# Kernel tuning notes

Measured on AMD Instinct MI355X. Metric: run time of the kernel, lower is better.

## Reference

```python
import jax, jax.numpy as jnp
import numpy as np

B, S, D, H, KS, VS, O = 4, 2048, 1024, 16, 64, 64, 1024


def setup_inputs() -> dict:
    key = jax.random.key(0)
    ks = jax.random.split(key, 11)
    def w(k, shp):
        return jax.random.normal(k, shp, dtype=jnp.float32) * 0.02
    return {
        "Q": jax.random.normal(ks[0], (B, S, D), dtype=jnp.float32),
        "K": jax.random.normal(ks[1], (B, S, D), dtype=jnp.float32),
        "V": jax.random.normal(ks[2], (B, S, D), dtype=jnp.float32),
        # per-head projection weights stacked over heads (equivalent to 3*H separate nn.Linear)
        "Wq": w(ks[3], (H, D, KS)), "bq": w(ks[4], (H, KS)),
        "Wk": w(ks[5], (H, D, KS)), "bk": w(ks[6], (H, KS)),
        "Wv": w(ks[7], (H, D, VS)), "bv": w(ks[8], (H, VS)),
        "Wo": w(ks[9], (H * VS, O)), "bo": w(ks[10], (O,)),
    }


def reference(Q, K, V, Wq, bq, Wk, bk, Wv, bv, Wo, bo):
    scale = jnp.sqrt(jnp.asarray(KS, dtype=Q.dtype))
    # per-head linear projections (vectorized over heads)
    q = jnp.einsum('bsd,hdk->bhsk', Q, Wq) + bq[:, None, :]   # [B,H,S,KS]
    k = jnp.einsum('bsd,hdk->bhsk', K, Wk) + bk[:, None, :]   # [B,H,S,KS]
    v = jnp.einsum('bsd,hdv->bhsv', V, Wv) + bv[:, None, :]   # [B,H,S,VS]
    # scaled dot-product attention, full S x S scores per head
    scores = jnp.einsum('bhsk,bhtk->bhst', q, k) / scale       # [B,H,S,S]
    attn = jax.nn.softmax(scores, axis=-1)
    heads = jnp.einsum('bhst,bhtv->bhsv', attn, v)             # [B,H,S,VS]
    # concat heads along feature dim -> [B,S,H*VS]
    cat = jnp.transpose(heads, (0, 2, 1, 3)).reshape(B, S, H * VS)
    return cat @ Wo + bo
```

## Files before the change

### kernel.cpp

```cpp
#include <hip/hip_runtime.h>
#include <hip/hip_fp16.h>
#include <cstdint>
#include <cstddef>

typedef _Float16 f16;
typedef _Float16 f16x8 __attribute__((ext_vector_type(8)));
typedef _Float16 f16x4 __attribute__((ext_vector_type(4)));
typedef float    f32x4 __attribute__((ext_vector_type(4)));

#define MFMA(a, b, c) __builtin_amdgcn_mfma_f32_16x16x32_f16(a, b, c, 0, 0, 0)


__device__ __forceinline__ void gload_lds16(const f16* g, f16* l) {
    __builtin_amdgcn_global_load_lds(
        (const __attribute__((address_space(1))) void*)g,
        (__attribute__((address_space(3))) void*)l, 16, 0, 0);
}

__global__ void k_convert3(const float* __restrict__ Q, const float* __restrict__ K,
                           const float* __restrict__ V, f16* __restrict__ Qh,
                           f16* __restrict__ Kh, f16* __restrict__ Vh) {
    const int seg = blockIdx.x >> 11;
    const int lb  = blockIdx.x & 2047;
    const float* src = seg == 0 ? Q : (seg == 1 ? K : V);
    f16* dst = seg == 0 ? Qh : (seg == 1 ? Kh : Vh);
    int i = lb * blockDim.x + threadIdx.x;
    for (; i < 2097152; i += 524288) {
        float4 v = ((const float4*)src)[i];
        f16x4 h;
        h[0] = (f16)v.x; h[1] = (f16)v.y; h[2] = (f16)v.z; h[3] = (f16)v.w;
        ((f16x4*)dst)[i] = h;
    }
}

__global__ void k_transpose_all(const float* __restrict__ Wq, const float* __restrict__ Wk,
                                const float* __restrict__ Wv, const float* __restrict__ Wo,
                                f16* __restrict__ WT, f16* __restrict__ WoT) {
    __shared__ float T[64][65];
    const int bx = blockIdx.x;
    const int widx = bx >> 8, sub = bx & 255;
    const int nb = sub >> 4, db = sub & 15;
    const int tid = threadIdx.x;
    const float* W = widx == 0 ? Wq : (widx == 1 ? Wk : (widx == 2 ? Wv : Wo));
    f16* Wt = (widx < 3) ? (WT + (size_t)widx * 1048576) : WoT;
    const float* src = (widx < 3) ? (W + nb * 65536 + db * 4096)
                                  : (W + db * 65536 + nb * 64);
    const int rstride = (widx < 3) ? 64 : 1024;
    {
        int nn = tid & 63, d0 = tid >> 6;
#pragma unroll
        for (int p = 0; p < 16; ++p) {
            int dd = p * 4 + d0;
            T[dd][nn] = src[dd * rstride + nn];
        }
    }
    __syncthreads();
    {
        int dd = tid & 63, n0 = tid >> 6;
#pragma unroll
        for (int p = 0; p < 16; ++p) {
            int nn = p * 4 + n0;
            Wt[(size_t)(nb * 64 + nn) * 1024 + db * 64 + dd] = (f16)T[dd][nn];
        }
    }
}

#define G256_STAGE(AD, BD, ASRC, BSRC, KT)                                      \
    do {                                                                        \
        int ktc = (KT);                                                         \
        _Pragma("unroll")                                                       \
        for (int i2 = 0; i2 < 4; ++i2) {                                        \
            int gA = wid * 4 + i2;                       \
            gload_lds16(&(ASRC)[(size_t)(row0 + gA * 8 + (lane >> 3)) * 1024    \
                                + ktc * 64 + (lane & 7) * 8],                   \
                        &(AD)[(gA * 68 + lane) * 8]);                           \
        }                                                                       \
        _Pragma("unroll")                                                       \
        for (int i2 = 0; i2 < 2; ++i2) {                                        \
            int gB = wid * 2 + i2;                                   \
            gload_lds16(&(BSRC)[(size_t)(col0 + gB * 8 + (lane >> 3)) * 1024    \
                                + ktc * 64 + (lane & 7) * 8],                   \
                        &(BD)[(gB * 68 + lane) * 8]);                           \
        }                                                                       \
    } while (0)

#define G256_COMPUTE(AB, BB)                                                    \
    do {                                                                        \
        _Pragma("unroll")                                                       \
        for (int kk = 0; kk < 2; ++kk) {                                        \
            f16x8 af[4], bf[4];                                                 \
            _Pragma("unroll")                                                   \
            for (int m = 0; m < 4; ++m) {                                       \
                int rw = wm * 64 + m * 16 + lr;                                 \
                af[m] = *(const f16x8*)&(AB)[((rw >> 3) * 68 + (rw & 7) * 8     \
                                              + kk * 4 + lg) * 8];              \
            }                                                                   \
            _Pragma("unroll")                                                   \
            for (int n = 0; n < 4; ++n) {                                       \
                int rw = wn * 64 + n * 16 + lr;                                 \
                bf[n] = *(const f16x8*)&(BB)[((rw >> 3) * 68 + (rw & 7) * 8     \
                                              + kk * 4 + lg) * 8];              \
            }                                                                   \
            _Pragma("unroll")                                                   \
            for (int m = 0; m < 4; ++m)                                         \
                _Pragma("unroll")                                               \
                for (int n = 0; n < 4; ++n)                                     \
                    acc[m][n] = MFMA(af[m], bf[n], acc[m][n]);                  \
        }                                                                       \
    } while (0)

#define G256_PIPELINE(ASRC, BSRC)                                              \
    int cur = 0, nx1 = 1, nx2 = 2;                                             \
    G256_STAGE(As3, Bs3, ASRC, BSRC, 0);                                       \
    for (int t = 0; t < 16; ++t) {                                             \
        int tn = t < 15 ? t + 1 : 15;                                          \
        G256_STAGE(As3 + nx1 * 17408, Bs3 + nx1 * 8704, ASRC, BSRC, tn);       \
        asm volatile("s_waitcnt vmcnt(6)" ::: "memory");                       \
        __builtin_amdgcn_sched_barrier(0);                                     \
        __builtin_amdgcn_s_barrier();                                          \
        __builtin_amdgcn_sched_barrier(0);                                     \
        const f16* Ab = As3 + cur * 17408;                                     \
        const f16* Bb = Bs3 + cur * 8704;                                      \
        G256_COMPUTE(Ab, Bb);                                                  \
        int tmp = cur; cur = nx1; nx1 = nx2; nx2 = tmp;                        \
    }

__global__ __launch_bounds__(512, 1) void k_gemm_qkv256(
    const f16* __restrict__ Qh, const f16* __restrict__ Kh, const f16* __restrict__ Vh,
    const f16* __restrict__ WT, const float* __restrict__ bq,
    const float* __restrict__ bk, const float* __restrict__ bv,
    f16* __restrict__ qout, f16* __restrict__ kout, f16* __restrict__ vout, float SC) {
    __shared__ f16 As3[3 * 17408];
    __shared__ f16 Bs3[3 * 8704];
    const int yy = blockIdx.y;
    const int seg = yy >> 3;
    const f16* A    = seg == 0 ? Qh : (seg == 1 ? Kh : Vh);
    const f16* Bt   = WT + (size_t)seg * 1048576;
    const float* bias = seg == 0 ? bq : (seg == 1 ? bk : bv);
    const float scale = seg == 0 ? SC : 1.0f;

    const int tid = threadIdx.x;
    const int wid = tid >> 6, lane = tid & 63;
    const int wm = wid >> 1, wn = wid & 1;
    const int lr = lane & 15, lg = lane >> 4;
    const int row0 = blockIdx.x * 256, col0 = (yy & 7) * 128;

    f32x4 acc[4][4];
#pragma unroll
    for (int m = 0; m < 4; ++m)
#pragma unroll
        for (int n = 0; n < 4; ++n) acc[m][n] = (f32x4){0.f, 0.f, 0.f, 0.f};

    G256_PIPELINE(A, Bt)

#pragma unroll
    for (int m = 0; m < 4; ++m) {
#pragma unroll
        for (int n = 0; n < 4; ++n) {
            int col = col0 + wn * 64 + n * 16 + lr;
            float bv_ = bias[col];
            int rowb = row0 + wm * 64 + m * 16 + lg * 4;
            int srow = rowb & 2047;
            if (seg == 0) {
#pragma unroll
                for (int r = 0; r < 4; ++r) {
                    int row = rowb + r;
                    size_t a = ((size_t)((row >> 11) * 16 + (col >> 6)) * 2048 + (row & 2047)) * 64 + (col & 63);
                    qout[a] = (f16)((acc[m][n][r] + bv_) * scale);
                }
            } else if (seg == 1) {
                int ks5 = srow & 31;
                int p0 = ((ks5 >> 2) & 1) * 16 + (ks5 >> 3) * 4 + (ks5 & 3);
                size_t abase = (size_t)((rowb >> 11) * 16 + (col >> 6)) * 131072
                             + (size_t)(srow >> 5) * 2048
                             + (size_t)(p0 >> 4) * 512
                             + (size_t)((col & 63) >> 5) * 1024
                             + (size_t)((col & 31) >> 3) * 128
                             + (col & 7);
#pragma unroll
                for (int r = 0; r < 4; ++r)
                    kout[abase + (size_t)((p0 & 15) + r) * 8] = (f16)(acc[m][n][r] + bv_);
            } else {
                size_t a = (size_t)((rowb >> 11) * 16 + (col >> 6)) * 131072
                         + (size_t)(srow >> 5) * 2048
                         + (size_t)((col & 63) >> 4) * 512
                         + (size_t)((srow & 31) >> 3) * 128
                         + (size_t)(col & 15) * 8
                         + (srow & 7);
                f16x4 ov;
#pragma unroll
                for (int r = 0; r < 4; ++r) ov[r] = (f16)(acc[m][n][r] + bv_);
                *(f16x4*)&vout[a] = ov;
            }
        }
    }
}

__global__ __launch_bounds__(512, 1) void k_gemm_out256(const f16* __restrict__ A,
                                                        const f16* __restrict__ Bt,
                                                        const float* __restrict__ bias,
                                                        float* __restrict__ Cout) {
    __shared__ f16 As3[3 * 17408];
    __shared__ f16 Bs3[3 * 8704];
    const int tid = threadIdx.x;
    const int wid = tid >> 6, lane = tid & 63;
    const int wm = wid >> 1, wn = wid & 1;
    const int lr = lane & 15, lg = lane >> 4;
    const int row0 = blockIdx.x * 256, col0 = blockIdx.y * 128;

    f32x4 acc[4][4];
#pragma unroll
    for (int m = 0; m < 4; ++m)
#pragma unroll
        for (int n = 0; n < 4; ++n) acc[m][n] = (f32x4){0.f, 0.f, 0.f, 0.f};

    G256_PIPELINE(A, Bt)

#pragma unroll
    for (int m = 0; m < 4; ++m) {
#pragma unroll
        for (int n = 0; n < 4; ++n) {
            int col = col0 + wn * 64 + n * 16 + lr;
            float bv = bias[col];
#pragma unroll
            for (int r = 0; r < 4; ++r) {
                int row = row0 + wm * 64 + m * 16 + lg * 4 + r;
                Cout[(size_t)row * 1024 + col] = acc[m][n][r] + bv;
            }
        }
    }
}

#define ATTN_TILE(Kc, Vc)                                                     \
    do {                                                                      \
        f16x8 ka0 = *(const f16x8*)&(Kc)[fo];                                 \
        f16x8 ka1 = *(const f16x8*)&(Kc)[fo + 1024];                          \
        f16x8 ka2 = *(const f16x8*)&(Kc)[fo + 512];                           \
        f16x8 ka3 = *(const f16x8*)&(Kc)[fo + 1536];                          \
        f32x4 st[2][2];                                                       \
        _Pragma("unroll")                                                     \
        for (int qt = 0; qt < 2; ++qt) {                                      \
            float nm = -m_r[qt];                                              \
            f32x4 z = (f32x4){nm, nm, nm, nm};                                \
            z = MFMA(ka0, qf[qt][0], z);                                      \
            z = MFMA(ka1, qf[qt][1], z);                                      \
            st[qt][0] = z;                                                    \
            f32x4 z2 = (f32x4){nm, nm, nm, nm};                               \
            z2 = MFMA(ka2, qf[qt][0], z2);                                    \
            z2 = MFMA(ka3, qf[qt][1], z2);                                    \
            st[qt][1] = z2;                                                   \
        }                                                                     \
        f16x8 vv0 = *(const f16x8*)&(Vc)[fo];                                 \
        f16x8 vv1 = *(const f16x8*)&(Vc)[fo + 512];                           \
        f16x8 vv2 = *(const f16x8*)&(Vc)[fo + 1024];                          \
        f16x8 vv3 = *(const f16x8*)&(Vc)[fo + 1536];                          \
        {                                                                     \
            float lm[2];                                                      \
            _Pragma("unroll")                                                 \
            for (int qt = 0; qt < 2; ++qt) {                                  \
                float a0 = fmaxf(fmaxf(st[qt][0][0], st[qt][0][1]), st[qt][0][2]); \
                float b0 = fmaxf(fmaxf(st[qt][0][3], st[qt][1][0]), st[qt][1][1]); \
                float c0 = fmaxf(fmaxf(st[qt][1][2], st[qt][1][3]), a0);      \
                lm[qt] = fmaxf(b0, c0);                                       \
            }                                                                 \
            if (__any((lm[0] > THR) || (lm[1] > THR))) {                      \
                _Pragma("unroll")                                             \
                for (int qt = 0; qt < 2; ++qt) {                              \
                    float t0 = lm[qt];                                        \
                    t0 = fmaxf(t0, __shfl_xor(t0, 16, 64));                   \
                    t0 = fmaxf(t0, __shfl_xor(t0, 32, 64));                   \
                    float delta = fmaxf(0.f, t0);                             \
                    float alpha = __builtin_amdgcn_exp2f(-delta);             \
                    _Pragma("unroll")                                         \
                    for (int m = 0; m < 4; ++m)                               \
                        _Pragma("unroll")                                     \
                        for (int r = 0; r < 4; ++r) o[qt][m][r] *= alpha;     \
                    l_p[qt] *= alpha;                                         \
                    m_r[qt] += delta;                                         \
                    _Pragma("unroll")                                         \
                    for (int t = 0; t < 2; ++t)                               \
                        _Pragma("unroll")                                     \
                        for (int r = 0; r < 4; ++r) st[qt][t][r] -= delta;    \
                }                                                             \
            }                                                                 \
        }                                                                     \
        f16x8 pf[2];                                                          \
        _Pragma("unroll")                                                     \
        for (int qt = 0; qt < 2; ++qt) {                                      \
            float ps = 0.f;                                                   \
            union { uint32_t u[4]; f16x8 v; } bb;                             \
            _Pragma("unroll")                                                 \
            for (int t = 0; t < 2; ++t)                                       \
                _Pragma("unroll")                                             \
                for (int pr = 0; pr < 2; ++pr) {                              \
                    float e0 = __builtin_amdgcn_exp2f(st[qt][t][2 * pr]);     \
                    float e1 = __builtin_amdgcn_exp2f(st[qt][t][2 * pr + 1]); \
                    ps += e0 + e1;                                            \
                    auto hp = __builtin_amdgcn_cvt_pkrtz(e0, e1);             \
                    bb.u[t * 2 + pr] = __builtin_bit_cast(uint32_t, hp);      \
                }                                                             \
            l_p[qt] += ps;                                                    \
            pf[qt] = bb.v;                                                    \
        }                                                                     \
        _Pragma("unroll")                                                     \
        for (int qt = 0; qt < 2; ++qt) {                                      \
            o[qt][0] = MFMA(vv0, pf[qt], o[qt][0]);                           \
            o[qt][1] = MFMA(vv1, pf[qt], o[qt][1]);                           \
            o[qt][2] = MFMA(vv2, pf[qt], o[qt][2]);                           \
            o[qt][3] = MFMA(vv3, pf[qt], o[qt][3]);                           \
        }                                                                     \
    } while (0)

__global__ __launch_bounds__(256, 4) void k_attn(const f16* __restrict__ q,
                                                 const f16* __restrict__ k2,
                                                 const f16* __restrict__ v2,
                                                 f16* __restrict__ cat) {
    const int g = blockIdx.x;
    const int xcd = g & 7, i = g >> 3;
    const int bh = xcd * 8 + (i >> 4);
    const int qb = i & 15;
    const int b = bh >> 4, h = bh & 15;

    const int tid = threadIdx.x, wid = tid >> 6, lane = tid & 63;
    const int lr = lane & 15, lg = lane >> 4;
    const int qw = qb * 128 + wid * 32;

    __shared__ f16 Ks[4][2048];
    __shared__ f16 Vs[4][2048];

    const float THR = 8.0f;

    f16x8 qf[2][2];
#pragma unroll
    for (int qt = 0; qt < 2; ++qt)
#pragma unroll
        for (int hf = 0; hf < 2; ++hf)
            qf[qt][hf] = *(const f16x8*)&q[((size_t)bh * 2048 + qw + qt * 16 + lr) * 64 + hf * 32 + lg * 8];

    const f16* kt = k2 + (size_t)bh * 131072;
    const f16* vt = v2 + (size_t)bh * 131072;
    const int so = tid * 8;
    const int fo = lane * 8;

    f32x4 o[2][4];
#pragma unroll
    for (int qt = 0; qt < 2; ++qt)
#pragma unroll
        for (int m = 0; m < 4; ++m) o[qt][m] = (f32x4){0.f, 0.f, 0.f, 0.f};
    float m_r[2] = {0.f, 0.f}, l_p[2] = {0.f, 0.f};

    gload_lds16(kt + so, &Ks[0][so]);
    gload_lds16(vt + so, &Vs[0][so]);
    gload_lds16(kt + 2048 + so, &Ks[1][so]);
    gload_lds16(vt + 2048 + so, &Vs[1][so]);
    __syncthreads();

    for (int pp = 0; pp < 32; ++pp) {
        const int t0 = 2 * pp;
        const int ba = t0 & 3, bb2 = (t0 + 1) & 3;
        const int bc = (t0 + 2) & 3, bd = (t0 + 3) & 3;

        gload_lds16(kt + (size_t)(t0 + 2) * 2048 + so, &Ks[bc][so]);
        gload_lds16(vt + (size_t)(t0 + 2) * 2048 + so, &Vs[bc][so]);
        gload_lds16(kt + (size_t)(t0 + 3) * 2048 + so, &Ks[bd][so]);
        gload_lds16(vt + (size_t)(t0 + 3) * 2048 + so, &Vs[bd][so]);

        ATTN_TILE(&Ks[ba][0], &Vs[ba][0]);
        ATTN_TILE(&Ks[bb2][0], &Vs[bb2][0]);

        __syncthreads();
    }

#pragma unroll
    for (int qt = 0; qt < 2; ++qt) {
        float l = l_p[qt];
        l += __shfl_xor(l, 16, 64);
        l += __shfl_xor(l, 32, 64);
        float inv = 1.f / l;
        size_t cb = ((size_t)b * 2048 + qw + qt * 16 + lr) * 1024 + h * 64 + lg * 4;
#pragma unroll
        for (int m = 0; m < 4; ++m) {
            f16x4 ov;
#pragma unroll
            for (int r = 0; r < 4; ++r) ov[r] = (f16)(o[qt][m][r] * inv);
            *(f16x4*)&cat[cb + m * 16] = ov;
        }
    }
}

extern "C" void kernel_launch(void* const* d_in, const int* in_sizes, int n_in,
                              void* d_out, int out_size, void* d_ws, size_t ws_size,
                              hipStream_t stream) {
    const float* Q  = (const float*)d_in[0];
    const float* K  = (const float*)d_in[1];
    const float* V  = (const float*)d_in[2];
    const float* Wq = (const float*)d_in[3];
    const float* bq = (const float*)d_in[4];
    const float* Wk = (const float*)d_in[5];
    const float* bk = (const float*)d_in[6];
    const float* Wv = (const float*)d_in[7];
    const float* bv = (const float*)d_in[8];
    const float* Wo = (const float*)d_in[9];
    const float* bo = (const float*)d_in[10];

    char* ws = (char*)d_ws;
    size_t off = 0;
    auto alloc = [&](size_t bytes) {
        char* p = ws + off;
        off += (bytes + 255) & ~(size_t)255;
        return p;
    };
    f16* Qh  = (f16*)alloc(8192ULL * 1024 * 2);
    f16* Kh  = (f16*)alloc(8192ULL * 1024 * 2);
    f16* Vh  = (f16*)alloc(8192ULL * 1024 * 2);
    f16* WT  = (f16*)alloc(3ULL * 1024 * 1024 * 2);
    f16* WoT = (f16*)alloc(1024ULL * 1024 * 2);
    f16* qb  = (f16*)alloc(8192ULL * 1024 * 2);
    f16* kb2 = (f16*)alloc(8192ULL * 1024 * 2);
    f16* vb2 = (f16*)alloc(8192ULL * 1024 * 2);
    f16* cat = (f16*)alloc(8192ULL * 1024 * 2);

    k_convert3<<<6144, 256, 0, stream>>>(Q, K, V, Qh, Kh, Vh);
    k_transpose_all<<<1024, 256, 0, stream>>>(Wq, Wk, Wv, Wo, WT, WoT);

    const float SC = 0.125f * 1.44269504089f;
    k_gemm_qkv256<<<dim3(32, 24), 512, 0, stream>>>(Qh, Kh, Vh, WT, bq, bk, bv,
                                                    qb, kb2, vb2, SC);

    k_attn<<<1024, 256, 0, stream>>>(qb, kb2, vb2, cat);

    k_gemm_out256<<<dim3(32, 8), 512, 0, stream>>>(cat, WoT, bo, (float*)d_out);
}
```

Baseline: 202.9 us.

## Split attention work to one 16-row query tile per wave with 512-thread blocks

Each wave of the attention kernel now handles a single 16-row query tile instead of two, and the block grows from 4 to 8 waves so each block still covers 128 queries. K/V tile loads into LDS are split so half the threads load K and half load V. The aim is to cut per-wave register use and raise occupancy and latency hiding. The cost is half the MFMA work per LDS fragment read, since K/V fragments are no longer reused across two query tiles, and more waves contend at each block barrier.

Result: no change. 203.0 us (+0.0%).

```diff
diff --git a/kernel.cpp b/kernel.cpp
--- a/kernel.cpp
+++ b/kernel.cpp
@@ -231,87 +231,74 @@
     }
 }
 
-#define ATTN_TILE(Kc, Vc)                                                     \
+#define ATTN_TILE1(Kc, Vc)                                                    \
     do {                                                                      \
         f16x8 ka0 = *(const f16x8*)&(Kc)[fo];                                 \
         f16x8 ka1 = *(const f16x8*)&(Kc)[fo + 1024];                          \
         f16x8 ka2 = *(const f16x8*)&(Kc)[fo + 512];                           \
         f16x8 ka3 = *(const f16x8*)&(Kc)[fo + 1536];                          \
-        f32x4 st[2][2];                                                       \
-        _Pragma("unroll")                                                     \
-        for (int qt = 0; qt < 2; ++qt) {                                      \
-            float nm = -m_r[qt];                                              \
+        f32x4 st0, st1;                                                       \
+        {                                                                     \
+            float nm = -m_r;                                                  \
             f32x4 z = (f32x4){nm, nm, nm, nm};                                \
-            z = MFMA(ka0, qf[qt][0], z);                                      \
-            z = MFMA(ka1, qf[qt][1], z);                                      \
-            st[qt][0] = z;                                                    \
+            z = MFMA(ka0, qf0, z);                                            \
+            z = MFMA(ka1, qf1, z);                                            \
+            st0 = z;                                                          \
             f32x4 z2 = (f32x4){nm, nm, nm, nm};                               \
-            z2 = MFMA(ka2, qf[qt][0], z2);                                    \
-            z2 = MFMA(ka3, qf[qt][1], z2);                                    \
-            st[qt][1] = z2;                                                   \
+            z2 = MFMA(ka2, qf0, z2);                                          \
+            z2 = MFMA(ka3, qf1, z2);                                          \
+            st1 = z2;                                                         \
         }                                                                     \
         f16x8 vv0 = *(const f16x8*)&(Vc)[fo];                                 \
         f16x8 vv1 = *(const f16x8*)&(Vc)[fo + 512];                           \
         f16x8 vv2 = *(const f16x8*)&(Vc)[fo + 1024];                          \
         f16x8 vv3 = *(const f16x8*)&(Vc)[fo + 1536];                          \
         {                                                                     \
-            float lm[2];                                                      \
-            _Pragma("unroll")                                                 \
-            for (int qt = 0; qt < 2; ++qt) {                                  \
-                float a0 = fmaxf(fmaxf(st[qt][0][0], st[qt][0][1]), st[qt][0][2]); \
-                float b0 = fmaxf(fmaxf(st[qt][0][3], st[qt][1][0]), st[qt][1][1]); \
-                float c0 = fmaxf(fmaxf(st[qt][1][2], st[qt][1][3]), a0);      \
-                lm[qt] = fmaxf(b0, c0);                                       \
-            }                                                                 \
-            if (__any((lm[0] > THR) || (lm[1] > THR))) {                      \
+            float a0 = fmaxf(fmaxf(st0[0], st0[1]), st0[2]);                  \
+            float b0 = fmaxf(fmaxf(st0[3], st1[0]), st1[1]);                  \
+            float c0 = fmaxf(fmaxf(st1[2], st1[3]), a0);                      \
+            float lm = fmaxf(b0, c0);                                         \
+            if (__any(lm > THR)) {                                            \
+                float t0v = lm;                                               \
+                t0v = fmaxf(t0v, __shfl_xor(t0v, 16, 64));                    \
+                t0v = fmaxf(t0v, __shfl_xor(t0v, 32, 64));                    \
+                float delta = fmaxf(0.f, t0v);                                \
+                float alpha = __builtin_amdgcn_exp2f(-delta);                 \
                 _Pragma("unroll")                                             \
-                for (int qt = 0; qt < 2; ++qt) {                              \
-                    float t0 = lm[qt];                                        \
-                    t0 = fmaxf(t0, __shfl_xor(t0, 16, 64));                   \
-                    t0 = fmaxf(t0, __shfl_xor(t0, 32, 64));                   \
-                    float delta = fmaxf(0.f, t0);                             \
-                    float alpha = __builtin_amdgcn_exp2f(-delta);             \
+                for (int m = 0; m < 4; ++m)                                   \
                     _Pragma("unroll")                                         \
-                    for (int m = 0; m < 4; ++m)                               \
-                        _Pragma("unroll")                                     \
-                        for (int r = 0; r < 4; ++r) o[qt][m][r] *= alpha;     \
-                    l_p[qt] *= alpha;                                         \
-                    m_r[qt] += delta;                                         \
-                    _Pragma("unroll")                                         \
-                    for (int t = 0; t < 2; ++t)                               \
-                        _Pragma("unroll")                                     \
-                        for (int r = 0; r < 4; ++r) st[qt][t][r] -= delta;    \
-                }                                                             \
+                    for (int r = 0; r < 4; ++r) o[m][r] *= alpha;             \
+                l_p *= alpha;                                                 \
+                m_r += delta;                                                 \
+                _Pragma("unroll")                                             \
+                for (int r = 0; r < 4; ++r) { st0[r] -= delta; st1[r] -= delta; } \
             }                                                                 \
         }                                                                     \
-        f16x8 pf[2];                                                          \
-        _Pragma("unroll")                                                     \
-        for (int qt = 0; qt < 2; ++qt) {                                      \
-            float ps = 0.f;                                                   \
+        f16x8 pf;                                                             \
+        {                                                                     \
             union { uint32_t u[4]; f16x8 v; } bb;                             \
-            _Pragma("unroll")                                                 \
-            for (int t = 0; t < 2; ++t)                                       \
-                _Pragma("unroll")                                             \
-                for (int pr = 0; pr < 2; ++pr) {                              \
-                    float e0 = __builtin_amdgcn_exp2f(st[qt][t][2 * pr]);     \
-                    float e1 = __builtin_amdgcn_exp2f(st[qt][t][2 * pr + 1]); \
-                    ps += e0 + e1;                                            \
-                    auto hp = __builtin_amdgcn_cvt_pkrtz(e0, e1);             \
-                    bb.u[t * 2 + pr] = __builtin_bit_cast(uint32_t, hp);      \
-                }                                                             \
-            l_p[qt] += ps;                                                    \
-            pf[qt] = bb.v;                                                    \
+            float e0 = __builtin_amdgcn_exp2f(st0[0]);                        \
+            float e1 = __builtin_amdgcn_exp2f(st0[1]);                        \
+            float e2 = __builtin_amdgcn_exp2f(st0[2]);                        \
+            float e3 = __builtin_amdgcn_exp2f(st0[3]);                        \
+            float e4 = __builtin_amdgcn_exp2f(st1[0]);                        \
+            float e5 = __builtin_amdgcn_exp2f(st1[1]);                        \
+            float e6 = __builtin_amdgcn_exp2f(st1[2]);                        \
+            float e7 = __builtin_amdgcn_exp2f(st1[3]);                        \
+            l_p += (e0 + e1) + (e2 + e3) + (e4 + e5) + (e6 + e7);             \
+            bb.u[0] = __builtin_bit_cast(uint32_t, __builtin_amdgcn_cvt_pkrtz(e0, e1)); \
+            bb.u[1] = __builtin_bit_cast(uint32_t, __builtin_amdgcn_cvt_pkrtz(e2, e3)); \
+            bb.u[2] = __builtin_bit_cast(uint32_t, __builtin_amdgcn_cvt_pkrtz(e4, e5)); \
+            bb.u[3] = __builtin_bit_cast(uint32_t, __builtin_amdgcn_cvt_pkrtz(e6, e7)); \
+            pf = bb.v;                                                        \
         }                                                                     \
-        _Pragma("unroll")                                                     \
-        for (int qt = 0; qt < 2; ++qt) {                                      \
-            o[qt][0] = MFMA(vv0, pf[qt], o[qt][0]);                           \
-            o[qt][1] = MFMA(vv1, pf[qt], o[qt][1]);                           \
-            o[qt][2] = MFMA(vv2, pf[qt], o[qt][2]);                           \
-            o[qt][3] = MFMA(vv3, pf[qt], o[qt][3]);                           \
-        }                                                                     \
+        o[0] = MFMA(vv0, pf, o[0]);                                           \
+        o[1] = MFMA(vv1, pf, o[1]);                                           \
+        o[2] = MFMA(vv2, pf, o[2]);                                           \
+        o[3] = MFMA(vv3, pf, o[3]);                                           \
     } while (0)
 
-__global__ __launch_bounds__(256, 4) void k_attn(const f16* __restrict__ q,
+__global__ __launch_bounds__(512, 8) void k_attn(const f16* __restrict__ q,
                                                  const f16* __restrict__ k2,
                                                  const f16* __restrict__ v2,
                                                  f16* __restrict__ cat) {
@@ -323,36 +310,34 @@
 
     const int tid = threadIdx.x, wid = tid >> 6, lane = tid & 63;
     const int lr = lane & 15, lg = lane >> 4;
-    const int qw = qb * 128 + wid * 32;
+    const int qw = qb * 128 + wid * 16;
 
     __shared__ f16 Ks[4][2048];
     __shared__ f16 Vs[4][2048];
 
     const float THR = 8.0f;
 
-    f16x8 qf[2][2];
-#pragma unroll
-    for (int qt = 0; qt < 2; ++qt)
-#pragma unroll
-        for (int hf = 0; hf < 2; ++hf)
-            qf[qt][hf] = *(const f16x8*)&q[((size_t)bh * 2048 + qw + qt * 16 + lr) * 64 + hf * 32 + lg * 8];
+    f16x8 qf0 = *(const f16x8*)&q[((size_t)bh * 2048 + qw + lr) * 64 + lg * 8];
+    f16x8 qf1 = *(const f16x8*)&q[((size_t)bh * 2048 + qw + lr) * 64 + 32 + lg * 8];
 
     const f16* kt = k2 + (size_t)bh * 131072;
     const f16* vt = v2 + (size_t)bh * 131072;
-    const int so = tid * 8;
+    const bool sgK = (tid < 256);
+    const int so2 = (tid & 255) * 8;
     const int fo = lane * 8;
 
-    f32x4 o[2][4];
-#pragma unroll
-    for (int qt = 0; qt < 2; ++qt)
-#pragma unroll
-        for (int m = 0; m < 4; ++m) o[qt][m] = (f32x4){0.f, 0.f, 0.f, 0.f};
-    float m_r[2] = {0.f, 0.f}, l_p[2] = {0.f, 0.f};
-
-    gload_lds16(kt + so, &Ks[0][so]);
-    gload_lds16(vt + so, &Vs[0][so]);
-    gload_lds16(kt + 2048 + so, &Ks[1][so]);
-    gload_lds16(vt + 2048 + so, &Vs[1][so]);
+    f32x4 o[4];
+#pragma unroll
+    for (int m = 0; m < 4; ++m) o[m] = (f32x4){0.f, 0.f, 0.f, 0.f};
+    float m_r = 0.f, l_p = 0.f;
+
+    if (sgK) {
+        gload_lds16(kt + so2, &Ks[0][so2]);
+        gload_lds16(kt + 2048 + so2, &Ks[1][so2]);
+    } else {
+        gload_lds16(vt + so2, &Vs[0][so2]);
+        gload_lds16(vt + 2048 + so2, &Vs[1][so2]);
+    }
     __syncthreads();
 
     for (int pp = 0; pp < 32; ++pp) {
@@ -360,29 +345,31 @@
         const int ba = t0 & 3, bb2 = (t0 + 1) & 3;
         const int bc = (t0 + 2) & 3, bd = (t0 + 3) & 3;
 
-        gload_lds16(kt + (size_t)(t0 + 2) * 2048 + so, &Ks[bc][so]);
-        gload_lds16(vt + (size_t)(t0 + 2) * 2048 + so, &Vs[bc][so]);
-        gload_lds16(kt + (size_t)(t0 + 3) * 2048 + so, &Ks[bd][so]);
-        gload_lds16(vt + (size_t)(t0 + 3) * 2048 + so, &Vs[bd][so]);
-
-        ATTN_TILE(&Ks[ba][0], &Vs[ba][0]);
-        ATTN_TILE(&Ks[bb2][0], &Vs[bb2][0]);
+        if (sgK) {
+            gload_lds16(kt + (size_t)(t0 + 2) * 2048 + so2, &Ks[bc][so2]);
+            gload_lds16(kt + (size_t)(t0 + 3) * 2048 + so2, &Ks[bd][so2]);
+        } else {
+            gload_lds16(vt + (size_t)(t0 + 2) * 2048 + so2, &Vs[bc][so2]);
+            gload_lds16(vt + (size_t)(t0 + 3) * 2048 + so2, &Vs[bd][so2]);
+        }
+
+        ATTN_TILE1(&Ks[ba][0], &Vs[ba][0]);
+        ATTN_TILE1(&Ks[bb2][0], &Vs[bb2][0]);
 
         __syncthreads();
     }
 
-#pragma unroll
-    for (int qt = 0; qt < 2; ++qt) {
-        float l = l_p[qt];
+    {
+        float l = l_p;
         l += __shfl_xor(l, 16, 64);
         l += __shfl_xor(l, 32, 64);
         float inv = 1.f / l;
-        size_t cb = ((size_t)b * 2048 + qw + qt * 16 + lr) * 1024 + h * 64 + lg * 4;
+        size_t cb = ((size_t)b * 2048 + qw + lr) * 1024 + h * 64 + lg * 4;
 #pragma unroll
         for (int m = 0; m < 4; ++m) {
             f16x4 ov;
 #pragma unroll
-            for (int r = 0; r < 4; ++r) ov[r] = (f16)(o[qt][m][r] * inv);
+            for (int r = 0; r < 4; ++r) ov[r] = (f16)(o[m][r] * inv);
             *(f16x4*)&cat[cb + m * 16] = ov;
         }
     }
@@ -427,7 +414,7 @@
     k_gemm_qkv256<<<dim3(32, 24), 512, 0, stream>>>(Qh, Kh, Vh, WT, bq, bk, bv,
                                                     qb, kb2, vb2, SC);
 
-    k_attn<<<1024, 256, 0, stream>>>(qb, kb2, vb2, cat);
+    k_attn<<<1024, 512, 0, stream>>>(qb, kb2, vb2, cat);
 
     k_gemm_out256<<<dim3(32, 8), 512, 0, stream>>>(cat, WoT, bo, (float*)d_out);
 }
```

## Split attention over two KV halves with 512-thread blocks and add merge kernel

Applied to the files above, without the earlier changes.

Rewrites the attention kernel flash-decoding style. Each block now handles 256 query rows with 8 waves over one half of the key/value sequence, writes unnormalized partial outputs plus running max and sum, and a new merge kernel combines the two halves into the concatenated head layout. The aim is to halve each block's serial KV loop and raise per-block parallelism, with K and V staging split across thread halves. The cost is an extra kernel launch, extra global traffic for partial outputs and statistics, and fp16 rounding of unnormalized partial outputs.

Result: slower. 492.0 us (+142.5%).

```diff
diff --git a/kernel.cpp b/kernel.cpp
--- a/kernel.cpp
+++ b/kernel.cpp
@@ -70,14 +70,14 @@
         int ktc = (KT);                                                         \
         _Pragma("unroll")                                                       \
         for (int i2 = 0; i2 < 4; ++i2) {                                        \
-            int gA = wid * 4 + i2;                       \
+            int gA = wid * 4 + i2;                                              \
             gload_lds16(&(ASRC)[(size_t)(row0 + gA * 8 + (lane >> 3)) * 1024    \
                                 + ktc * 64 + (lane & 7) * 8],                   \
                         &(AD)[(gA * 68 + lane) * 8]);                           \
         }                                                                       \
         _Pragma("unroll")                                                       \
         for (int i2 = 0; i2 < 2; ++i2) {                                        \
-            int gB = wid * 2 + i2;                                   \
+            int gB = wid * 2 + i2;                                              \
             gload_lds16(&(BSRC)[(size_t)(col0 + gB * 8 + (lane >> 3)) * 1024    \
                                 + ktc * 64 + (lane & 7) * 8],                   \
                         &(BD)[(gB * 68 + lane) * 8]);                           \
@@ -266,10 +266,10 @@
             if (__any((lm[0] > THR) || (lm[1] > THR))) {                      \
                 _Pragma("unroll")                                             \
                 for (int qt = 0; qt < 2; ++qt) {                              \
-                    float t0 = lm[qt];                                        \
-                    t0 = fmaxf(t0, __shfl_xor(t0, 16, 64));                   \
-                    t0 = fmaxf(t0, __shfl_xor(t0, 32, 64));                   \
-                    float delta = fmaxf(0.f, t0);                             \
+                    float t0v = lm[qt];                                       \
+                    t0v = fmaxf(t0v, __shfl_xor(t0v, 16, 64));                \
+                    t0v = fmaxf(t0v, __shfl_xor(t0v, 32, 64));                \
+                    float delta = fmaxf(0.f, t0v);                            \
                     float alpha = __builtin_amdgcn_exp2f(-delta);             \
                     _Pragma("unroll")                                         \
                     for (int m = 0; m < 4; ++m)                               \
@@ -311,19 +311,22 @@
         }                                                                     \
     } while (0)
 
-__global__ __launch_bounds__(256, 4) void k_attn(const f16* __restrict__ q,
-                                                 const f16* __restrict__ k2,
-                                                 const f16* __restrict__ v2,
-                                                 f16* __restrict__ cat) {
+__global__ __launch_bounds__(512, 6) void k_attn_part(const f16* __restrict__ q,
+                                                      const f16* __restrict__ k2,
+                                                      const f16* __restrict__ v2,
+                                                      f16* __restrict__ po,
+                                                      float* __restrict__ sm,
+                                                      float* __restrict__ sl) {
     const int g = blockIdx.x;
     const int xcd = g & 7, i = g >> 3;
     const int bh = xcd * 8 + (i >> 4);
-    const int qb = i & 15;
-    const int b = bh >> 4, h = bh & 15;
+    const int rr = i & 15;
+    const int qb = rr & 7;
+    const int ks = rr >> 3;
 
     const int tid = threadIdx.x, wid = tid >> 6, lane = tid & 63;
     const int lr = lane & 15, lg = lane >> 4;
-    const int qw = qb * 128 + wid * 32;
+    const int qw = qb * 256 + wid * 32;
 
     __shared__ f16 Ks[4][2048];
     __shared__ f16 Vs[4][2048];
@@ -337,9 +340,10 @@
         for (int hf = 0; hf < 2; ++hf)
             qf[qt][hf] = *(const f16x8*)&q[((size_t)bh * 2048 + qw + qt * 16 + lr) * 64 + hf * 32 + lg * 8];
 
-    const f16* kt = k2 + (size_t)bh * 131072;
-    const f16* vt = v2 + (size_t)bh * 131072;
-    const int so = tid * 8;
+    const f16* kt = k2 + (size_t)bh * 131072 + (size_t)ks * 65536;
+    const f16* vt = v2 + (size_t)bh * 131072 + (size_t)ks * 65536;
+    const bool sgK = (tid < 256);
+    const int so2 = (tid & 255) * 8;
     const int fo = lane * 8;
 
     f32x4 o[2][4];
@@ -349,21 +353,27 @@
         for (int m = 0; m < 4; ++m) o[qt][m] = (f32x4){0.f, 0.f, 0.f, 0.f};
     float m_r[2] = {0.f, 0.f}, l_p[2] = {0.f, 0.f};
 
-    gload_lds16(kt + so, &Ks[0][so]);
-    gload_lds16(vt + so, &Vs[0][so]);
-    gload_lds16(kt + 2048 + so, &Ks[1][so]);
-    gload_lds16(vt + 2048 + so, &Vs[1][so]);
+    if (sgK) {
+        gload_lds16(kt + so2, &Ks[0][so2]);
+        gload_lds16(kt + 2048 + so2, &Ks[1][so2]);
+    } else {
+        gload_lds16(vt + so2, &Vs[0][so2]);
+        gload_lds16(vt + 2048 + so2, &Vs[1][so2]);
+    }
     __syncthreads();
 
-    for (int pp = 0; pp < 32; ++pp) {
+    for (int pp = 0; pp < 16; ++pp) {
         const int t0 = 2 * pp;
         const int ba = t0 & 3, bb2 = (t0 + 1) & 3;
         const int bc = (t0 + 2) & 3, bd = (t0 + 3) & 3;
 
-        gload_lds16(kt + (size_t)(t0 + 2) * 2048 + so, &Ks[bc][so]);
-        gload_lds16(vt + (size_t)(t0 + 2) * 2048 + so, &Vs[bc][so]);
-        gload_lds16(kt + (size_t)(t0 + 3) * 2048 + so, &Ks[bd][so]);
-        gload_lds16(vt + (size_t)(t0 + 3) * 2048 + so, &Vs[bd][so]);
+        if (sgK) {
+            gload_lds16(kt + (size_t)(t0 + 2) * 2048 + so2, &Ks[bc][so2]);
+            gload_lds16(kt + (size_t)(t0 + 3) * 2048 + so2, &Ks[bd][so2]);
+        } else {
+            gload_lds16(vt + (size_t)(t0 + 2) * 2048 + so2, &Vs[bc][so2]);
+            gload_lds16(vt + (size_t)(t0 + 3) * 2048 + so2, &Vs[bd][so2]);
+        }
 
         ATTN_TILE(&Ks[ba][0], &Vs[ba][0]);
         ATTN_TILE(&Ks[bb2][0], &Vs[bb2][0]);
@@ -376,16 +386,43 @@
         float l = l_p[qt];
         l += __shfl_xor(l, 16, 64);
         l += __shfl_xor(l, 32, 64);
-        float inv = 1.f / l;
-        size_t cb = ((size_t)b * 2048 + qw + qt * 16 + lr) * 1024 + h * 64 + lg * 4;
+        int R = bh * 2048 + qw + qt * 16 + lr;
+        size_t pb = ((size_t)ks * 131072 + R) * 64 + lg * 4;
 #pragma unroll
         for (int m = 0; m < 4; ++m) {
             f16x4 ov;
 #pragma unroll
-            for (int r = 0; r < 4; ++r) ov[r] = (f16)(o[qt][m][r] * inv);
-            *(f16x4*)&cat[cb + m * 16] = ov;
-        }
-    }
+            for (int r = 0; r < 4; ++r) ov[r] = (f16)o[qt][m][r];
+            *(f16x4*)&po[pb + m * 16] = ov;
+        }
+        if (lg == 0) {
+            sm[ks * 131072 + R] = m_r[qt];
+            sl[ks * 131072 + R] = l;
+        }
+    }
+}
+
+__global__ void k_merge(const f16* __restrict__ po, const float* __restrict__ sm,
+                        const float* __restrict__ sl, f16* __restrict__ cat) {
+    const int tid = threadIdx.x;
+    const int R = blockIdx.x * 32 + (tid >> 3);
+    const int vd8 = (tid & 7) * 8;
+    const int bh = R >> 11, srow = R & 2047;
+    const int b = bh >> 4, h = bh & 15;
+    float m0 = sm[R], m1 = sm[131072 + R];
+    float l0 = sl[R], l1 = sl[131072 + R];
+    float M = fmaxf(m0, m1);
+    float w0 = __builtin_amdgcn_exp2f(m0 - M);
+    float w1 = __builtin_amdgcn_exp2f(m1 - M);
+    float inv = 1.f / (l0 * w0 + l1 * w1);
+    w0 *= inv; w1 *= inv;
+    f16x8 p0 = *(const f16x8*)&po[(size_t)R * 64 + vd8];
+    f16x8 p1 = *(const f16x8*)&po[((size_t)131072 + R) * 64 + vd8];
+    f16x8 outv;
+#pragma unroll
+    for (int j = 0; j < 8; ++j)
+        outv[j] = (f16)((float)p0[j] * w0 + (float)p1[j] * w1);
+    *(f16x8*)&cat[((size_t)b * 2048 + srow) * 1024 + h * 64 + vd8] = outv;
 }
 
 extern "C" void kernel_launch(void* const* d_in, const int* in_sizes, int n_in,
@@ -419,6 +456,9 @@
     f16* kb2 = (f16*)alloc(8192ULL * 1024 * 2);
     f16* vb2 = (f16*)alloc(8192ULL * 1024 * 2);
     f16* cat = (f16*)alloc(8192ULL * 1024 * 2);
+    f16* po  = (f16*)alloc(2ULL * 131072 * 64 * 2);
+    float* sm = (float*)alloc(2ULL * 131072 * 4);
+    float* sl = (float*)alloc(2ULL * 131072 * 4);
 
     k_convert3<<<6144, 256, 0, stream>>>(Q, K, V, Qh, Kh, Vh);
     k_transpose_all<<<1024, 256, 0, stream>>>(Wq, Wk, Wv, Wo, WT, WoT);
@@ -427,7 +467,8 @@
     k_gemm_qkv256<<<dim3(32, 24), 512, 0, stream>>>(Qh, Kh, Vh, WT, bq, bk, bv,
                                                     qb, kb2, vb2, SC);
 
-    k_attn<<<1024, 256, 0, stream>>>(qb, kb2, vb2, cat);
+    k_attn_part<<<1024, 512, 0, stream>>>(qb, kb2, vb2, po, sm, sl);
+    k_merge<<<4096, 256, 0, stream>>>(po, sm, sl, cat);
 
     k_gemm_out256<<<dim3(32, 8), 512, 0, stream>>>(cat, WoT, bo, (float*)d_out);
 }
```

## Double attention block size to 8 waves sharing each K/V tile

Applied to the files above, without the earlier changes.

The attention kernel now launches 512-thread blocks covering 256 query rows instead of 128, with half the grid. Each staged K/V tile in shared memory is reused by twice as many query waves, which halves global K/V traffic per query. The loading threads are split so the first 256 load K and the rest load V. The trade-off is fewer blocks (512 across the GPU) and larger synchronization groups, which may reduce occupancy and latency hiding. Launch bounds of 512x4 may also constrain registers.

After: 193.5 us. -4.6%, faster.

```diff
diff --git a/kernel.cpp b/kernel.cpp
--- a/kernel.cpp
+++ b/kernel.cpp
@@ -70,14 +70,14 @@
         int ktc = (KT);                                                         \
         _Pragma("unroll")                                                       \
         for (int i2 = 0; i2 < 4; ++i2) {                                        \
-            int gA = wid * 4 + i2;                       \
+            int gA = wid * 4 + i2;                                              \
             gload_lds16(&(ASRC)[(size_t)(row0 + gA * 8 + (lane >> 3)) * 1024    \
                                 + ktc * 64 + (lane & 7) * 8],                   \
                         &(AD)[(gA * 68 + lane) * 8]);                           \
         }                                                                       \
         _Pragma("unroll")                                                       \
         for (int i2 = 0; i2 < 2; ++i2) {                                        \
-            int gB = wid * 2 + i2;                                   \
+            int gB = wid * 2 + i2;                                              \
             gload_lds16(&(BSRC)[(size_t)(col0 + gB * 8 + (lane >> 3)) * 1024    \
                                 + ktc * 64 + (lane & 7) * 8],                   \
                         &(BD)[(gB * 68 + lane) * 8]);                           \
@@ -266,10 +266,10 @@
             if (__any((lm[0] > THR) || (lm[1] > THR))) {                      \
                 _Pragma("unroll")                                             \
                 for (int qt = 0; qt < 2; ++qt) {                              \
-                    float t0 = lm[qt];                                        \
-                    t0 = fmaxf(t0, __shfl_xor(t0, 16, 64));                   \
-                    t0 = fmaxf(t0, __shfl_xor(t0, 32, 64));                   \
-                    float delta = fmaxf(0.f, t0);                             \
+                    float t0v = lm[qt];                                       \
+                    t0v = fmaxf(t0v, __shfl_xor(t0v, 16, 64));                \
+                    t0v = fmaxf(t0v, __shfl_xor(t0v, 32, 64));                \
+                    float delta = fmaxf(0.f, t0v);                            \
                     float alpha = __builtin_amdgcn_exp2f(-delta);             \
                     _Pragma("unroll")                                         \
                     for (int m = 0; m < 4; ++m)                               \
@@ -311,19 +311,19 @@
         }                                                                     \
     } while (0)
 
-__global__ __launch_bounds__(256, 4) void k_attn(const f16* __restrict__ q,
+__global__ __launch_bounds__(512, 4) void k_attn(const f16* __restrict__ q,
                                                  const f16* __restrict__ k2,
                                                  const f16* __restrict__ v2,
                                                  f16* __restrict__ cat) {
     const int g = blockIdx.x;
     const int xcd = g & 7, i = g >> 3;
-    const int bh = xcd * 8 + (i >> 4);
-    const int qb = i & 15;
+    const int bh = xcd * 8 + (i >> 3);
+    const int qb = i & 7;
     const int b = bh >> 4, h = bh & 15;
 
     const int tid = threadIdx.x, wid = tid >> 6, lane = tid & 63;
     const int lr = lane & 15, lg = lane >> 4;
-    const int qw = qb * 128 + wid * 32;
+    const int qw = qb * 256 + wid * 32;
 
     __shared__ f16 Ks[4][2048];
     __shared__ f16 Vs[4][2048];
@@ -339,7 +339,8 @@
 
     const f16* kt = k2 + (size_t)bh * 131072;
     const f16* vt = v2 + (size_t)bh * 131072;
-    const int so = tid * 8;
+    const bool sgK = (tid < 256);
+    const int so2 = (tid & 255) * 8;
     const int fo = lane * 8;
 
     f32x4 o[2][4];
@@ -349,10 +350,13 @@
         for (int m = 0; m < 4; ++m) o[qt][m] = (f32x4){0.f, 0.f, 0.f, 0.f};
     float m_r[2] = {0.f, 0.f}, l_p[2] = {0.f, 0.f};
 
-    gload_lds16(kt + so, &Ks[0][so]);
-    gload_lds16(vt + so, &Vs[0][so]);
-    gload_lds16(kt + 2048 + so, &Ks[1][so]);
-    gload_lds16(vt + 2048 + so, &Vs[1][so]);
+    if (sgK) {
+        gload_lds16(kt + so2, &Ks[0][so2]);
+        gload_lds16(kt + 2048 + so2, &Ks[1][so2]);
+    } else {
+        gload_lds16(vt + so2, &Vs[0][so2]);
+        gload_lds16(vt + 2048 + so2, &Vs[1][so2]);
+    }
     __syncthreads();
 
     for (int pp = 0; pp < 32; ++pp) {
@@ -360,10 +364,13 @@
         const int ba = t0 & 3, bb2 = (t0 + 1) & 3;
         const int bc = (t0 + 2) & 3, bd = (t0 + 3) & 3;
 
-        gload_lds16(kt + (size_t)(t0 + 2) * 2048 + so, &Ks[bc][so]);
-        gload_lds16(vt + (size_t)(t0 + 2) * 2048 + so, &Vs[bc][so]);
-        gload_lds16(kt + (size_t)(t0 + 3) * 2048 + so, &Ks[bd][so]);
-        gload_lds16(vt + (size_t)(t0 + 3) * 2048 + so, &Vs[bd][so]);
+        if (sgK) {
+            gload_lds16(kt + (size_t)(t0 + 2) * 2048 + so2, &Ks[bc][so2]);
+            gload_lds16(kt + (size_t)(t0 + 3) * 2048 + so2, &Ks[bd][so2]);
+        } else {
+            gload_lds16(vt + (size_t)(t0 + 2) * 2048 + so2, &Vs[bc][so2]);
+            gload_lds16(vt + (size_t)(t0 + 3) * 2048 + so2, &Vs[bd][so2]);
+        }
 
         ATTN_TILE(&Ks[ba][0], &Vs[ba][0]);
         ATTN_TILE(&Ks[bb2][0], &Vs[bb2][0]);
@@ -427,7 +434,7 @@
     k_gemm_qkv256<<<dim3(32, 24), 512, 0, stream>>>(Qh, Kh, Vh, WT, bq, bk, bv,
                                                     qb, kb2, vb2, SC);
 
-    k_attn<<<1024, 256, 0, stream>>>(qb, kb2, vb2, cat);
+    k_attn<<<512, 512, 0, stream>>>(qb, kb2, vb2, cat);
 
     k_gemm_out256<<<dim3(32, 8), 512, 0, stream>>>(cat, WoT, bo, (float*)d_out);
 }
```
